# Kernel tuning notes

Hardware: AMD Instinct MI355X
Metric: run time of the kernel (lower is better)

Reference implementation:

```python
import jax, jax.numpy as jnp
import numpy as np

DIM = 1024
NUM_HEADS = 16
HEAD_DIM = DIM // NUM_HEADS
SCALE = HEAD_DIM ** -0.5
ETA = 1e-5


def setup_inputs() -> dict:
    key = jax.random.key(0)
    ks = jax.random.split(key, 5)
    B, N = 4, 2048
    x = jax.random.normal(ks[0], (B, N, DIM), dtype=jnp.float32)
    # weights stored [in, out] for x @ W
    W_qkv = jax.random.normal(ks[1], (DIM, 3 * DIM), dtype=jnp.float32) * (DIM ** -0.5)
    gamma1 = jnp.full((3 * DIM,), ETA, dtype=jnp.float32)
    W_proj = jax.random.normal(ks[2], (DIM, DIM), dtype=jnp.float32) * (DIM ** -0.5)
    b_proj = jnp.zeros((DIM,), dtype=jnp.float32)
    gamma2 = jnp.full((DIM,), ETA, dtype=jnp.float32)
    return {"x": x, "W_qkv": W_qkv, "gamma1": gamma1, "W_proj": W_proj,
            "b_proj": b_proj, "gamma2": gamma2}


def reference(x, W_qkv, gamma1, W_proj, b_proj, gamma2):
    B, N, C = x.shape
    H, D = NUM_HEADS, HEAD_DIM
    # qkv projection (no bias), layerscaled by gamma1 before head split
    qkv = (x @ W_qkv) * gamma1                      # [B, N, 3C]
    qkv = qkv.reshape(B, N, 3, H, D)
    q = qkv[:, :, 0].transpose(0, 2, 1, 3)          # [B, H, N, D]
    k = qkv[:, :, 1].transpose(0, 2, 1, 3)
    v = qkv[:, :, 2].transpose(0, 2, 1, 3)
    attn = jnp.einsum('bhnd,bhmd->bhnm', q, k) * SCALE
    attn = jax.nn.softmax(attn, axis=-1)
    out = jnp.einsum('bhnm,bhmd->bhnd', attn, v)    # [B, H, N, D]
    out = out.transpose(0, 2, 1, 3).reshape(B, N, C)
    return gamma2 * (out @ W_proj + b_proj)
```

## Files before the change

kernel.cpp:

```cpp
#include <hip/hip_runtime.h>

#define DIM 1024
#define NHEADS 16
#define HDIM 64
#define BATCH 4
#define SEQ 2048
#define MTOT (BATCH*SEQ)
#define QSC 0.18033688011112042f
#define KVB 64
#define NT (SEQ/KVB)
#define PSTR_B 144
#define DEFER_THR 8.0f

typedef __bf16 bf16;
typedef __bf16 bf16x8 __attribute__((ext_vector_type(8)));
typedef __bf16 bf16x4 __attribute__((ext_vector_type(4)));
typedef float  f32x4  __attribute__((ext_vector_type(4)));

static __device__ __forceinline__ bf16 f2bf(float f) {
  unsigned u = __builtin_bit_cast(unsigned, f);
  u = (u + 0x7FFFu + ((u >> 16) & 1u)) >> 16;
  unsigned short s = (unsigned short)u;
  return __builtin_bit_cast(bf16, s);
}

static __device__ __forceinline__ float exp2g(float x) {
#if __has_builtin(__builtin_amdgcn_exp2f)
  return __builtin_amdgcn_exp2f(x);
#else
  float r; asm("v_exp_f32 %0, %1" : "=v"(r) : "v"(x)); return r;
#endif
}

#define GLD16(gp, lp) __builtin_amdgcn_global_load_lds( \
    (const __attribute__((address_space(1))) void*)(gp), \
    (__attribute__((address_space(3))) void*)(lp), 16, 0, 0)

__global__ __launch_bounds__(256) void k_cvt_x(const float* __restrict__ x,
                                               bf16* __restrict__ xb) {
  size_t i = ((size_t)blockIdx.x * 256 + threadIdx.x) * 4;
  const float4 v = *(const float4*)(x + i);
  bf16x4 o;
  o[0] = f2bf(v.x); o[1] = f2bf(v.y); o[2] = f2bf(v.z); o[3] = f2bf(v.w);
  *(bf16x4*)(xb + i) = o;
}

__global__ __launch_bounds__(256) void k_prep_w(const float* __restrict__ W,
                                                const float* __restrict__ sc,
                                                bf16* __restrict__ Wt,
                                                int C, int qscale) {
  __shared__ float tile[32][33];
  const int tx = threadIdx.x, ty = threadIdx.y;
  const int c0 = blockIdx.x * 32, k0 = blockIdx.y * 32;
#pragma unroll
  for (int j = 0; j < 4; ++j)
    tile[ty + 8*j][tx] = W[(size_t)(k0 + ty + 8*j) * C + (c0 + tx)];
  __syncthreads();
#pragma unroll
  for (int j = 0; j < 4; ++j) {
    int cc = c0 + ty + 8*j;
    float s = sc[cc];
    if (qscale && cc < DIM) s *= QSC;
    Wt[(size_t)cc * DIM + (k0 + tx)] = f2bf(tile[tx][ty + 8*j] * s);
  }
}

template<int MODE>
__global__ __launch_bounds__(256) void k_gemm(const bf16* __restrict__ A,
                                              const bf16* __restrict__ Bt,
                                              int nblk,
                                              float* __restrict__ outp,
                                              const float* __restrict__ g2,
                                              const float* __restrict__ bp,
                                              bf16* __restrict__ Qb,
                                              bf16* __restrict__ Kb,
                                              bf16* __restrict__ Vb) {
  __shared__ bf16 Als[128*32];
  __shared__ bf16 Bls[128*32];
  const int b0 = blockIdx.x;
  const int bswz = (b0 & 7) * ((int)gridDim.x >> 3) + (b0 >> 3);
  const int bm = bswz / nblk, bn = bswz % nblk;
  const int t = threadIdx.x;
  const int lane = t & 63, wave = t >> 6;
  const int c = lane & 15, g = lane >> 4;
  const int wm = (wave >> 1) * 64, wn = (wave & 1) * 64;
  const int srow = t >> 2, schunk = t & 3;
  const bf16* Ab = A  + (size_t)(bm*128) * DIM;
  const bf16* Bb = Bt + (size_t)(bn*128) * DIM;
  f32x4 acc[4][4] = {};
  for (int k0 = 0; k0 < DIM; k0 += 32) {
    __syncthreads();
#pragma unroll
    for (int i = 0; i < 2; ++i) {
      GLD16(Ab + (size_t)(i*64 + srow)*DIM + k0 + schunk*8,
            (char*)Als + i*4096 + t*16);
      GLD16(Bb + (size_t)(i*64 + srow)*DIM + k0 + schunk*8,
            (char*)Bls + i*4096 + t*16);
    }
    __syncthreads();
    bf16x8 a[4], b[4];
#pragma unroll
    for (int m = 0; m < 4; ++m)
      a[m] = *(const bf16x8*)&Als[(wm + m*16 + c)*32 + g*8];
#pragma unroll
    for (int n = 0; n < 4; ++n)
      b[n] = *(const bf16x8*)&Bls[(wn + n*16 + c)*32 + g*8];
#pragma unroll
    for (int m = 0; m < 4; ++m)
#pragma unroll
      for (int n = 0; n < 4; ++n)
        acc[m][n] = __builtin_amdgcn_mfma_f32_16x16x32_bf16(a[m], b[n], acc[m][n], 0, 0, 0);
  }
  const int cb = bn*128 + wn, rb = bm*128 + wm;
  if (MODE == 0) {
    const int which = (bn*128) >> 10;
    if (which < 2) {
      bf16* dst = which == 0 ? Qb : Kb;
#pragma unroll
      for (int n = 0; n < 4; ++n) {
        const int colg = cb + n*16 + c;
        const int h = (colg >> 6) & 15, d = colg & 63;
        const size_t hd = (size_t)h * (SEQ*HDIM) + d;
#pragma unroll
        for (int m = 0; m < 4; ++m)
#pragma unroll
          for (int r = 0; r < 4; ++r) {
            const int row = rb + m*16 + 4*g + r;
            const int bb = row >> 11, nt = row & 2047;
            dst[(size_t)bb * (NHEADS*SEQ*HDIM) + hd + (size_t)nt * HDIM] = (bf16)acc[m][n][r];
          }
      }
    } else {
#pragma unroll
      for (int n = 0; n < 4; ++n) {
        const int colg = cb + n*16 + c;
        const int h = (colg >> 6) & 15, d = colg & 63;
#pragma unroll
        for (int m = 0; m < 4; ++m) {
          const int row0 = rb + m*16 + 4*g;
          const int bb = row0 >> 11, nt = row0 & 2047;
          bf16x4 pk;
          pk[0] = (bf16)acc[m][n][0]; pk[1] = (bf16)acc[m][n][1];
          pk[2] = (bf16)acc[m][n][2]; pk[3] = (bf16)acc[m][n][3];
          *(bf16x4*)(Vb + ((size_t)(bb*NHEADS + h)*HDIM + d)*SEQ + nt) = pk;
        }
      }
    }
  } else {
#pragma unroll
    for (int n = 0; n < 4; ++n) {
      const int col = cb + n*16 + c;
      const float bias = g2[col] * bp[col];
#pragma unroll
      for (int m = 0; m < 4; ++m)
#pragma unroll
        for (int r = 0; r < 4; ++r) {
          const int row = rb + m*16 + 4*g + r;
          outp[(size_t)row * DIM + col] = acc[m][n][r] + bias;
        }
    }
  }
}

__global__ __launch_bounds__(512, 4) void k_attn(const bf16* __restrict__ Q,
                                                 const bf16* __restrict__ K,
                                                 const bf16* __restrict__ Vt,
                                                 bf16* __restrict__ O) {
  __shared__ __align__(16) char Kls[2][KVB*128];
  __shared__ __align__(16) char Vls[2][KVB*128];
  __shared__ __align__(16) char Ones[16*128];
  __shared__ __align__(16) char Pls[8][32*PSTR_B];
  const int b0 = blockIdx.x;
  const int bid = (b0 & 7) * 64 + (b0 >> 3);
  const int qt = bid & 7, bh = bid >> 3;
  const int t = threadIdx.x, wave = t >> 6, lane = t & 63;
  const int c = lane & 15, g = lane >> 4;
  const int csw = (c & 7) << 4;
  char* Pw = Pls[wave];
  const bf16* Qp = Q + ((size_t)bh * SEQ + qt*256) * HDIM;
  const bf16* Kp = K + (size_t)bh * SEQ * HDIM;
  const bf16* Vh = Vt + (size_t)bh * HDIM * SEQ;
  {
    unsigned fill = (t*4 < 128) ? 0x3F803F80u : 0u;
    *(unsigned*)(Ones + t*4) = fill;
  }
  bf16x8 qf[2][2];
#pragma unroll
  for (int m = 0; m < 2; ++m)
#pragma unroll
    for (int kk = 0; kk < 2; ++kk)
      qf[m][kk] = *(const bf16x8*)(Qp + (size_t)(wave*32 + m*16 + c)*HDIM + kk*32 + g*8);
  f32x4 oacc[2][5] = {};
  float rm[2] = {-1e30f, -1e30f};

  const int srow = t >> 3, scbk = t & 7;
#define STAGE(buf, kv0) { \
  GLD16(Kp + (size_t)((kv0) + srow)*HDIM + 8*(scbk ^ (srow & 7)), Kls[buf] + t*16); \
  GLD16(Vh + (size_t)srow*SEQ + (kv0) + 8*(scbk ^ (srow & 7)), Vls[buf] + t*16); }

  STAGE(0, 0);
  __syncthreads();
  int cur = 0;
  for (int tile = 0; tile < NT; ++tile) {
    if (tile + 1 < NT) STAGE(cur ^ 1, (tile + 1)*KVB);
    f32x4 s2[4][2] = {};
#pragma unroll
    for (int kk = 0; kk < 2; ++kk)
#pragma unroll
      for (int n = 0; n < 4; ++n) {
        const bf16x8 kb = *(const bf16x8*)(Kls[cur] + (n*16 + c)*128 + ((kk*64 + 16*g) ^ csw));
#pragma unroll
        for (int m = 0; m < 2; ++m)
          s2[n][m] = __builtin_amdgcn_mfma_f32_16x16x32_bf16(kb, qf[m][kk], s2[n][m], 0, 0, 0);
      }
    float pm[2];
    bool allok = true;
#pragma unroll
    for (int m = 0; m < 2; ++m) {
      float v = s2[0][m][0];
#pragma unroll
      for (int n = 0; n < 4; ++n)
#pragma unroll
        for (int r = 0; r < 4; ++r) v = fmaxf(v, s2[n][m][r]);
      pm[m] = v;
      allok = allok && (v <= rm[m] + DEFER_THR);
    }
    if (tile == 0 || !__all((int)allok)) {
#pragma unroll
      for (int m = 0; m < 2; ++m) {
        float v = pm[m];
        v = fmaxf(v, __shfl_xor(v, 16));
        v = fmaxf(v, __shfl_xor(v, 32));
        const float mnew = fmaxf(rm[m], v);
        const float alpha = exp2g(rm[m] - mnew);
        rm[m] = mnew;
#pragma unroll
        for (int df = 0; df < 5; ++df) {
          oacc[m][df][0] *= alpha; oacc[m][df][1] *= alpha;
          oacc[m][df][2] *= alpha; oacc[m][df][3] *= alpha;
        }
      }
    }
#pragma unroll
    for (int m = 0; m < 2; ++m)
#pragma unroll
      for (int n = 0; n < 4; ++n) {
        bf16x4 pk;
#pragma unroll
        for (int r = 0; r < 4; ++r) pk[r] = (bf16)exp2g(s2[n][m][r] - rm[m]);
        *(bf16x4*)(Pw + (m*16 + c)*PSTR_B + n*32 + g*8) = pk;
      }
#pragma unroll
    for (int kf = 0; kf < 2; ++kf) {
      bf16x8 pbm[2];
#pragma unroll
      for (int m = 0; m < 2; ++m)
        pbm[m] = *(const bf16x8*)(Pw + (m*16 + c)*PSTR_B + kf*64 + 16*g);
#pragma unroll
      for (int df = 0; df < 5; ++df) {
        const bf16x8 va = (df < 4)
          ? *(const bf16x8*)(Vls[cur] + (df*16 + c)*128 + ((kf*64 + 16*g) ^ csw))
          : *(const bf16x8*)(Ones + c*128 + ((kf*64 + 16*g) ^ csw));
#pragma unroll
        for (int m = 0; m < 2; ++m)
          oacc[m][df] = __builtin_amdgcn_mfma_f32_16x16x32_bf16(va, pbm[m], oacc[m][df], 0, 0, 0);
      }
    }
    __syncthreads();
    cur ^= 1;
  }
#undef STAGE
  const int b = bh >> 4, h = bh & 15;
#pragma unroll
  for (int m = 0; m < 2; ++m) {
    const float lq = __shfl(oacc[m][4][0], c, 64);
    const float inv = 1.0f / lq;
    const int qg = qt*256 + wave*32 + m*16 + c;
    bf16* orow = O + ((size_t)b*SEQ + qg)*DIM + h*HDIM;
#pragma unroll
    for (int df = 0; df < 4; ++df)
#pragma unroll
      for (int r = 0; r < 4; ++r)
        orow[df*16 + 4*g + r] = (bf16)(oacc[m][df][r] * inv);
  }
}

extern "C" void kernel_launch(void* const* d_in, const int* in_sizes, int n_in,
                              void* d_out, int out_size, void* d_ws, size_t ws_size,
                              hipStream_t stream) {
  const float* x    = (const float*)d_in[0];
  const float* Wqkv = (const float*)d_in[1];
  const float* g1   = (const float*)d_in[2];
  const float* Wp   = (const float*)d_in[3];
  const float* bp   = (const float*)d_in[4];
  const float* g2   = (const float*)d_in[5];
  float* out = (float*)d_out;
  char* ws = (char*)d_ws;
  bf16* xb  = (bf16*)ws;
  bf16* Wqt = (bf16*)(ws + (16u<<20));
  bf16* Wpt = (bf16*)(ws + (22u<<20));
  bf16* Qb  = (bf16*)(ws + (24u<<20));
  bf16* Kb  = (bf16*)(ws + (40u<<20));
  bf16* Vb  = (bf16*)(ws + (56u<<20));

  k_cvt_x<<<(MTOT*DIM)/1024, 256, 0, stream>>>(x, xb);
  k_prep_w<<<dim3(96, 32), dim3(32, 8), 0, stream>>>(Wqkv, g1, Wqt, 3*DIM, 1);
  k_prep_w<<<dim3(32, 32), dim3(32, 8), 0, stream>>>(Wp, g2, Wpt, DIM, 0);
  k_gemm<0><<<64*24, 256, 0, stream>>>(xb, Wqt, 24, nullptr, nullptr, nullptr, Qb, Kb, Vb);
  k_attn<<<512, 512, 0, stream>>>(Qb, Kb, Vb, xb);
  k_gemm<1><<<64*8, 256, 0, stream>>>(xb, Wpt, 8, out, g2, bp, nullptr, nullptr, nullptr);
}
```

Measured before the change: 279.3 us.

## Replace QKV GEMM with 256x256-tile double-buffered pipelined kernel

Adds a dedicated QKV projection kernel using 256x256 output tiles with 512 threads and a 128KB LDS double buffer. The next K-slab's global-to-LDS loads are interleaved with MFMA work through explicit waitcnt, barriers and setprio. The aim is more data reuse per tile and load latency hidden behind compute, in place of the 128x128 single-buffered loop. The tradeoff is high LDS use (one block per CU) and only 384 blocks, which raises wave-quantization and occupancy risk. The old MODE 0 path is removed from the generic GEMM.

```diff
diff --git a/kernel.cpp b/kernel.cpp
--- a/kernel.cpp
+++ b/kernel.cpp
@@ -65,16 +65,109 @@
   }
 }
 
+__global__ __launch_bounds__(512, 2) void k_gemm256(const bf16* __restrict__ A,
+                                                    const bf16* __restrict__ Bt,
+                                                    bf16* __restrict__ Qb,
+                                                    bf16* __restrict__ Kb,
+                                                    bf16* __restrict__ Vb) {
+  __shared__ __align__(16) char LS[131072];
+  const int b0 = blockIdx.x;
+  const int bswz = (b0 & 7) * 48 + (b0 >> 3);
+  const int bm = bswz / 12, bn = bswz % 12;
+  const int t = threadIdx.x;
+  const int lane = t & 63, wave = t >> 6;
+  const int c = lane & 15, g = lane >> 4;
+  const int wr = wave >> 2, wc = wave & 3;
+  const bf16* Asrc = A  + (size_t)(bm*256 + (t >> 2)) * DIM + (t & 3) * 8;
+  const bf16* Bsrc = Bt + (size_t)(bn*256 + (t >> 2)) * DIM + (t & 3) * 8;
+  const int aoff = wr*8192 + c*64 + g*16;
+  const int boff = 16384 + wc*4096 + c*64 + g*16;
+
+  f32x4 acc[8][4] = {};
+
+#define PIECE(pp, kt, dset) { \
+    const int op_ = ((pp) >> 1) & 1, hf_ = (pp) & 1; \
+    const bf16* s_ = (op_ ? Bsrc : Asrc) + (size_t)(hf_*128)*DIM + (kt)*32; \
+    GLD16(s_, LS + (dset)*65536 + ((kt) & 1)*32768 + op_*16384 + hf_*8192 + t*16); }
+
+#pragma unroll
+  for (int p = 0; p < 8; ++p) PIECE(p, (p >> 2), 0);
+  __syncthreads();
+
+  for (int j = 0; j < 16; ++j) {
+    const int s = j & 1;
+    const char* sbase = LS + s*65536;
+#pragma unroll
+    for (int p = 0; p < 8; ++p) {
+      if (j < 15) PIECE(p, 2*(j+1) + (p >> 2), s ^ 1);
+      if (p == 3 || p == 7) {
+        asm volatile("s_waitcnt vmcnt(3)" ::: "memory");
+        __builtin_amdgcn_sched_barrier(0);
+      }
+      __builtin_amdgcn_s_barrier();
+      const int ks = p >> 2, qm = (p >> 1) & 1, qn = p & 1;
+      const char* ab = sbase + ks*32768 + qm*4096 + aoff;
+      const char* bb = sbase + ks*32768 + qn*2048 + boff;
+      bf16x8 af[4], bfr[2];
+#pragma unroll
+      for (int m = 0; m < 4; ++m) af[m] = *(const bf16x8*)(ab + m*1024);
+#pragma unroll
+      for (int n = 0; n < 2; ++n) bfr[n] = *(const bf16x8*)(bb + n*1024);
+      __builtin_amdgcn_s_setprio(1);
+#pragma unroll
+      for (int m = 0; m < 4; ++m)
+#pragma unroll
+        for (int n = 0; n < 2; ++n)
+          acc[qm*4 + m][qn*2 + n] = __builtin_amdgcn_mfma_f32_16x16x32_bf16(
+              af[m], bfr[n], acc[qm*4 + m][qn*2 + n], 0, 0, 0);
+      __builtin_amdgcn_s_setprio(0);
+      __builtin_amdgcn_s_barrier();
+    }
+  }
+#undef PIECE
+  const int which = (bn * 256) >> 10;
+  const int rb = bm*256 + wr*128, cb = bn*256 + wc*64;
+  if (which < 2) {
+    bf16* dst = which == 0 ? Qb : Kb;
+#pragma unroll
+    for (int n = 0; n < 4; ++n) {
+      const int colg = cb + n*16 + c;
+      const int h = (colg >> 6) & 15, d = colg & 63;
+      const size_t hd = (size_t)h * (SEQ*HDIM) + d;
+#pragma unroll
+      for (int m = 0; m < 8; ++m)
+#pragma unroll
+        for (int r = 0; r < 4; ++r) {
+          const int row = rb + m*16 + 4*g + r;
+          const int bb_ = row >> 11, nt = row & 2047;
+          dst[(size_t)bb_ * (NHEADS*SEQ*HDIM) + hd + (size_t)nt * HDIM] = (bf16)acc[m][n][r];
+        }
+    }
+  } else {
+#pragma unroll
+    for (int n = 0; n < 4; ++n) {
+      const int colg = cb + n*16 + c;
+      const int h = (colg >> 6) & 15, d = colg & 63;
+#pragma unroll
+      for (int m = 0; m < 8; ++m) {
+        const int row0 = rb + m*16 + 4*g;
+        const int bb_ = row0 >> 11, nt = row0 & 2047;
+        bf16x4 pk;
+        pk[0] = (bf16)acc[m][n][0]; pk[1] = (bf16)acc[m][n][1];
+        pk[2] = (bf16)acc[m][n][2]; pk[3] = (bf16)acc[m][n][3];
+        *(bf16x4*)(Vb + ((size_t)(bb_*NHEADS + h)*HDIM + d)*SEQ + nt) = pk;
+      }
+    }
+  }
+}
+
 template<int MODE>
 __global__ __launch_bounds__(256) void k_gemm(const bf16* __restrict__ A,
                                               const bf16* __restrict__ Bt,
                                               int nblk,
                                               float* __restrict__ outp,
                                               const float* __restrict__ g2,
-                                              const float* __restrict__ bp,
-                                              bf16* __restrict__ Qb,
-                                              bf16* __restrict__ Kb,
-                                              bf16* __restrict__ Vb) {
+                                              const float* __restrict__ bp) {
   __shared__ bf16 Als[128*32];
   __shared__ bf16 Bls[128*32];
   const int b0 = blockIdx.x;
@@ -112,53 +205,17 @@
         acc[m][n] = __builtin_amdgcn_mfma_f32_16x16x32_bf16(a[m], b[n], acc[m][n], 0, 0, 0);
   }
   const int cb = bn*128 + wn, rb = bm*128 + wm;
-  if (MODE == 0) {
-    const int which = (bn*128) >> 10;
-    if (which < 2) {
-      bf16* dst = which == 0 ? Qb : Kb;
-#pragma unroll
-      for (int n = 0; n < 4; ++n) {
-        const int colg = cb + n*16 + c;
-        const int h = (colg >> 6) & 15, d = colg & 63;
-        const size_t hd = (size_t)h * (SEQ*HDIM) + d;
-#pragma unroll
-        for (int m = 0; m < 4; ++m)
-#pragma unroll
-          for (int r = 0; r < 4; ++r) {
-            const int row = rb + m*16 + 4*g + r;
-            const int bb = row >> 11, nt = row & 2047;
-            dst[(size_t)bb * (NHEADS*SEQ*HDIM) + hd + (size_t)nt * HDIM] = (bf16)acc[m][n][r];
-          }
-      }
-    } else {
-#pragma unroll
-      for (int n = 0; n < 4; ++n) {
-        const int colg = cb + n*16 + c;
-        const int h = (colg >> 6) & 15, d = colg & 63;
-#pragma unroll
-        for (int m = 0; m < 4; ++m) {
-          const int row0 = rb + m*16 + 4*g;
-          const int bb = row0 >> 11, nt = row0 & 2047;
-          bf16x4 pk;
-          pk[0] = (bf16)acc[m][n][0]; pk[1] = (bf16)acc[m][n][1];
-          pk[2] = (bf16)acc[m][n][2]; pk[3] = (bf16)acc[m][n][3];
-          *(bf16x4*)(Vb + ((size_t)(bb*NHEADS + h)*HDIM + d)*SEQ + nt) = pk;
-        }
-      }
-    }
-  } else {
-#pragma unroll
-    for (int n = 0; n < 4; ++n) {
-      const int col = cb + n*16 + c;
-      const float bias = g2[col] * bp[col];
-#pragma unroll
-      for (int m = 0; m < 4; ++m)
-#pragma unroll
-        for (int r = 0; r < 4; ++r) {
-          const int row = rb + m*16 + 4*g + r;
-          outp[(size_t)row * DIM + col] = acc[m][n][r] + bias;
-        }
-    }
+#pragma unroll
+  for (int n = 0; n < 4; ++n) {
+    const int col = cb + n*16 + c;
+    const float bias = g2[col] * bp[col];
+#pragma unroll
+    for (int m = 0; m < 4; ++m)
+#pragma unroll
+      for (int r = 0; r < 4; ++r) {
+        const int row = rb + m*16 + 4*g + r;
+        outp[(size_t)row * DIM + col] = acc[m][n][r] + bias;
+      }
   }
 }
 
@@ -306,7 +363,7 @@
   k_cvt_x<<<(MTOT*DIM)/1024, 256, 0, stream>>>(x, xb);
   k_prep_w<<<dim3(96, 32), dim3(32, 8), 0, stream>>>(Wqkv, g1, Wqt, 3*DIM, 1);
   k_prep_w<<<dim3(32, 32), dim3(32, 8), 0, stream>>>(Wp, g2, Wpt, DIM, 0);
-  k_gemm<0><<<64*24, 256, 0, stream>>>(xb, Wqt, 24, nullptr, nullptr, nullptr, Qb, Kb, Vb);
+  k_gemm256<<<384, 512, 0, stream>>>(xb, Wqt, Qb, Kb, Vb);
   k_attn<<<512, 512, 0, stream>>>(Qb, Kb, Vb, xb);
-  k_gemm<1><<<64*8, 256, 0, stream>>>(xb, Wpt, 8, out, g2, bp, nullptr, nullptr, nullptr);
-}
+  k_gemm<1><<<64*8, 256, 0, stream>>>(xb, Wpt, 8, out, g2, bp);
+}
```

New measurement: 296.7 us. 6.3% more time.
